# Kernel optimization log

Hardware: AMD Instinct MI355X
Metric: run time of the kernel (lower is better)

The kernel has to match this reference:

```python
import jax, jax.numpy as jnp
import numpy as np


def _perm_mats():
    E = np.zeros((36, 9), np.float32)
    D = np.zeros((9, 36), np.float32)
    c = 0
    for i in range(8):
        for j in range(i + 1, 9):
            E[c, i] = 1.0
            E[c, j] = 1.0
            D[i, c] = 1.0
            D[j, c] = 1.0
            c += 1
    assert c == 36
    return E, D


def setup_inputs() -> dict:
    key = jax.random.key(0)
    B = 32768
    # binary candidate mask: [B, 9 digits, 9 rows, 9 cols]
    mask = jnp.round(jax.random.uniform(key, (B, 9, 9, 9), dtype=jnp.float32))
    E, D = _perm_mats()
    return {"mask": mask, "enc": jnp.asarray(E), "dec": jnp.asarray(D)}


def _nn_compare(x, v):
    # NNCompare: triangular bump == 1 exactly when x == v (for integer-valued x)
    return jnp.minimum(jax.nn.relu(x - (v - 1.0)), jax.nn.relu((v + 1.0) - x))


def _nn_and(x, y):
    return jnp.clip(jnp.minimum(x, y), 0.0, 1.0)


def reference(mask, enc, dec):
    B = mask.shape[0]
    # encode_permutations: 1x1 conv 9 -> 36 (pair selection)
    perms = jnp.einsum('oc,bchw->bohw', enc, mask)          # [B,36,9,9]
    perms = _nn_compare(perms, 2.0)                          # cell contains exactly this pair
    # sum_all_permutations: 1x1 conv 36 -> 1, then == 1
    sum_p = _nn_compare(jnp.sum(perms, axis=1, keepdims=True), 1.0)  # [B,1,9,9]
    perms = _nn_and(perms, sum_p)                            # broadcast over 36 channels
    # box downsample: grouped 3x3 stride-3 sum conv
    down = perms.reshape(B, 36, 3, 3, 3, 3).sum(axis=(3, 5))  # [B,36,3,3]
    down = _nn_compare(down, 2.0)                              # exactly two such cells in box
    up = jnp.repeat(jnp.repeat(down, 3, axis=2), 3, axis=3)    # [B,36,9,9]
    up = _nn_and(up, 1.0 - perms)                              # other cells in the box
    # decode_permutations: 1x1 conv 36 -> 9
    erase = jnp.einsum('oc,bchw->bohw', dec, up)               # [B,9,9,9]
    return _nn_and(mask, 1.0 - erase)
```

## Files before the change

### kernel.cpp

```cpp
#include <hip/hip_runtime.h>
#include <stdint.h>


#define NB 8
#define NFLOAT (NB * 729)
#define NVEC (NFLOAT / 4)
#define NCELL (NB * 81)
#define NBOX (NB * 9)
#define CPT 3
#define VPT 6

typedef float floatx4 __attribute__((ext_vector_type(4)));

__global__ __launch_bounds__(256) void sudoku_naked_pair_kernel(
    const float* __restrict__ mask, float* __restrict__ out) {
  __shared__ __align__(16) float buf[NFLOAT];
  __shared__ unsigned short pairm[NCELL];
  __shared__ unsigned short erls[NCELL];

  const int tid = threadIdx.x;
  const size_t base = (size_t)blockIdx.x * NFLOAT;

  floatx4 v[VPT];
#pragma unroll
  for (int i = 0; i < VPT; ++i) {
    const int idx = tid + i * 256;
    if (idx < NVEC)
      v[i] = *reinterpret_cast<const floatx4*>(mask + base + (size_t)idx * 4);
  }
#pragma unroll
  for (int i = 0; i < VPT; ++i) {
    const int idx = tid + i * 256;
    if (idx < NVEC)
      *reinterpret_cast<floatx4*>(buf + idx * 4) = v[i];
  }
  __syncthreads();

  uint32_t mycell[CPT];
#pragma unroll
  for (int it = 0; it < CPT; ++it) {
    const int c = tid + it * 256;
    if (c < NCELL) {
      const int b = c / 81, cell = c - b * 81;
      const float* p = buf + b * 729 + cell;
      uint32_t m = 0;
#pragma unroll
      for (int d = 0; d < 9; ++d) m |= (p[d * 81] != 0.0f ? 1u : 0u) << d;
      mycell[it] = m;
      pairm[c] = (unsigned short)((__popc(m) == 2) ? m : 0u);
    }
  }
  __syncthreads();

  if (tid < NBOX) {
    const int b = tid / 9, bi = tid - b * 9;
    const int bb = b * 81 + (bi / 3) * 27 + (bi % 3) * 3;
    uint32_t pm[9];
#pragma unroll
    for (int j = 0; j < 3; ++j) {
      pm[3 * j + 0] = pairm[bb + 9 * j + 0];
      pm[3 * j + 1] = pairm[bb + 9 * j + 1];
      pm[3 * j + 2] = pairm[bb + 9 * j + 2];
    }
    bool naked[9];
#pragma unroll
    for (int j = 0; j < 9; ++j) {
      int cnt = 0;
#pragma unroll
      for (int k = 0; k < 9; ++k) cnt += (pm[k] == pm[j]);
      naked[j] = (pm[j] != 0u) && (cnt == 2);
    }
#pragma unroll
    for (int j = 0; j < 9; ++j) {
      uint32_t er = 0;
#pragma unroll
      for (int k = 0; k < 9; ++k)
        if (naked[k] && pm[k] != pm[j]) er |= pm[k];
      const int cell = bb + 9 * (j / 3) + (j % 3);
      erls[cell] = (unsigned short)er;
    }
  }
  __syncthreads();

#pragma unroll
  for (int it = 0; it < CPT; ++it) {
    const int c = tid + it * 256;
    if (c < NCELL) {
      const int b = c / 81, cell = c - b * 81;
      const uint32_t fin = mycell[it] & ~(uint32_t)erls[c];
      float* q = buf + b * 729 + cell;
#pragma unroll
      for (int d = 0; d < 9; ++d) q[d * 81] = (float)((fin >> d) & 1u);
    }
  }
  __syncthreads();

#pragma unroll
  for (int i = 0; i < VPT; ++i) {
    const int idx = tid + i * 256;
    if (idx < NVEC) {
      const floatx4 w = *reinterpret_cast<const floatx4*>(buf + idx * 4);
      __builtin_nontemporal_store(
          w, reinterpret_cast<floatx4*>(out + base + (size_t)idx * 4));
    }
  }
}

extern "C" void kernel_launch(void* const* d_in, const int* in_sizes, int n_in,
                              void* d_out, int out_size, void* d_ws, size_t ws_size,
                              hipStream_t stream) {
  const float* mask = (const float*)d_in[0];
  float* out = (float*)d_out;
  const int B = in_sizes[0] / 729;
  const int grid = B / NB;
  sudoku_naked_pair_kernel<<<grid, 256, 0, stream>>>(mask, out);
}
```

Baseline: 177.5 us.

## Process four tiles per block with register prefetch of the next tile

```diff
diff --git a/kernel.cpp b/kernel.cpp
--- a/kernel.cpp
+++ b/kernel.cpp
@@ -9,32 +9,36 @@
 #define NBOX (NB * 9)
 #define CPT 3
 #define VPT 6
+#define TPB 4
 
 typedef float floatx4 __attribute__((ext_vector_type(4)));
 
-__global__ __launch_bounds__(256) void sudoku_naked_pair_kernel(
-    const float* __restrict__ mask, float* __restrict__ out) {
-  __shared__ __align__(16) float buf[NFLOAT];
-  __shared__ unsigned short pairm[NCELL];
-  __shared__ unsigned short erls[NCELL];
+__device__ __forceinline__ void lds_barrier() {
+  asm volatile("s_waitcnt lgkmcnt(0)" ::: "memory");
+  __builtin_amdgcn_s_barrier();
+  __builtin_amdgcn_sched_barrier(0);
+}
 
-  const int tid = threadIdx.x;
-  const size_t base = (size_t)blockIdx.x * NFLOAT;
-
-  floatx4 v[VPT];
+__device__ __forceinline__ void process_tile(
+    const float* __restrict__ mask, float* __restrict__ out,
+    float* buf, unsigned short* pairm, unsigned short* erls,
+    const int tid, const size_t tbase, const size_t next_base,
+    floatx4 (&vcur)[VPT], floatx4 (&vnext)[VPT], const bool prefetch) {
 #pragma unroll
   for (int i = 0; i < VPT; ++i) {
     const int idx = tid + i * 256;
     if (idx < NVEC)
-      v[i] = *reinterpret_cast<const floatx4*>(mask + base + (size_t)idx * 4);
+      *reinterpret_cast<floatx4*>(buf + idx * 4) = vcur[i];
   }
+  if (prefetch) {
 #pragma unroll
-  for (int i = 0; i < VPT; ++i) {
-    const int idx = tid + i * 256;
-    if (idx < NVEC)
-      *reinterpret_cast<floatx4*>(buf + idx * 4) = v[i];
+    for (int i = 0; i < VPT; ++i) {
+      const int idx = tid + i * 256;
+      if (idx < NVEC)
+        vnext[i] = *reinterpret_cast<const floatx4*>(mask + next_base + (size_t)idx * 4);
+    }
   }
-  __syncthreads();
+  lds_barrier();
 
   uint32_t mycell[CPT];
 #pragma unroll
@@ -50,7 +54,7 @@
       pairm[c] = (unsigned short)((__popc(m) == 2) ? m : 0u);
     }
   }
-  __syncthreads();
+  lds_barrier();
 
   if (tid < NBOX) {
     const int b = tid / 9, bi = tid - b * 9;
@@ -80,7 +84,7 @@
       erls[cell] = (unsigned short)er;
     }
   }
-  __syncthreads();
+  lds_barrier();
 
 #pragma unroll
   for (int it = 0; it < CPT; ++it) {
@@ -93,7 +97,7 @@
       for (int d = 0; d < 9; ++d) q[d * 81] = (float)((fin >> d) & 1u);
     }
   }
-  __syncthreads();
+  lds_barrier();
 
 #pragma unroll
   for (int i = 0; i < VPT; ++i) {
@@ -101,9 +105,41 @@
     if (idx < NVEC) {
       const floatx4 w = *reinterpret_cast<const floatx4*>(buf + idx * 4);
       __builtin_nontemporal_store(
-          w, reinterpret_cast<floatx4*>(out + base + (size_t)idx * 4));
+          w, reinterpret_cast<floatx4*>(out + tbase + (size_t)idx * 4));
     }
   }
+  lds_barrier();
+}
+
+__global__ __launch_bounds__(256) void sudoku_naked_pair_kernel(
+    const float* __restrict__ mask, float* __restrict__ out) {
+  __shared__ __align__(16) float buf[NFLOAT];
+  __shared__ unsigned short pairm[NCELL];
+  __shared__ unsigned short erls[NCELL];
+
+  const int tid = threadIdx.x;
+  const size_t tile0 = (size_t)blockIdx.x * TPB;
+
+  floatx4 va[VPT], vb[VPT];
+
+  {
+    const size_t b0 = tile0 * NFLOAT;
+#pragma unroll
+    for (int i = 0; i < VPT; ++i) {
+      const int idx = tid + i * 256;
+      if (idx < NVEC)
+        va[i] = *reinterpret_cast<const floatx4*>(mask + b0 + (size_t)idx * 4);
+    }
+  }
+
+  process_tile(mask, out, buf, pairm, erls, tid,
+               (tile0 + 0) * NFLOAT, (tile0 + 1) * NFLOAT, va, vb, true);
+  process_tile(mask, out, buf, pairm, erls, tid,
+               (tile0 + 1) * NFLOAT, (tile0 + 2) * NFLOAT, vb, va, true);
+  process_tile(mask, out, buf, pairm, erls, tid,
+               (tile0 + 2) * NFLOAT, (tile0 + 3) * NFLOAT, va, vb, true);
+  process_tile(mask, out, buf, pairm, erls, tid,
+               (tile0 + 3) * NFLOAT, (tile0 + 3) * NFLOAT, vb, va, false);
 }
 
 extern "C" void kernel_launch(void* const* d_in, const int* in_sizes, int n_in,
@@ -112,6 +148,7 @@
   const float* mask = (const float*)d_in[0];
   float* out = (float*)d_out;
   const int B = in_sizes[0] / 729;
-  const int grid = B / NB;
+  const int ntiles = B / NB;
+  const int grid = ntiles / TPB;
   sudoku_naked_pair_kernel<<<grid, 256, 0, stream>>>(mask, out);
 }
```

After: 183.7 us. +3.5%, slower.
